# Optimization experiments

Measured on AMD Instinct MI355X. Metric: run time of the kernel, lower is better.

The kernel has to match this reference:

```python
import jax, jax.numpy as jnp
import numpy as np

VOCAB = 1_000_000
EMB = 64
HID = 200
BATCH = 16384
FIELDS = 50
EPS = 1e-5


def batchnorm(x, gamma, beta):
    # training-mode BatchNorm1d: batch statistics, biased variance
    mean = jnp.mean(x, axis=0, keepdims=True)
    var = jnp.var(x, axis=0, keepdims=True)
    return (x - mean) * jax.lax.rsqrt(var + EPS) * gamma + beta


def setup_inputs() -> dict:
    key = jax.random.key(0)
    ks = jax.random.split(key, 9)
    x = jax.random.randint(ks[0], (BATCH, FIELDS), 0, VOCAB)
    emb = jax.random.normal(ks[1], (VOCAB, EMB), dtype=jnp.float32) * 0.01
    w1 = jax.random.normal(ks[2], (EMB, HID), dtype=jnp.float32) * (1.0 / np.sqrt(EMB))
    b1 = jnp.zeros((HID,), dtype=jnp.float32)
    w_last = jax.random.normal(ks[3], (HID, 1), dtype=jnp.float32) * (1.0 / np.sqrt(HID))
    b_last = jnp.zeros((1,), dtype=jnp.float32)
    g_bi = jnp.ones((EMB,), dtype=jnp.float32)
    be_bi = jnp.zeros((EMB,), dtype=jnp.float32)
    g_h = jnp.ones((HID,), dtype=jnp.float32)
    be_h = jnp.zeros((HID,), dtype=jnp.float32)
    return {"x": x, "emb": emb, "w1": w1, "b1": b1, "w_last": w_last,
            "b_last": b_last, "g_bi": g_bi, "be_bi": be_bi, "g_h": g_h, "be_h": be_h}


def reference(x, emb, w1, b1, w_last, b_last, g_bi, be_bi, g_h, be_h):
    e = emb[x]                                # [B, F, E] gather
    # sum_{i<j} e_i * e_j == 0.5 * ((sum e)^2 - sum e^2)  (FM identity)
    s = jnp.sum(e, axis=1)                    # [B, E]
    sq = jnp.sum(e * e, axis=1)               # [B, E]
    bi = 0.5 * (s * s - sq)                   # [B, E]
    h = jax.nn.relu(batchnorm(bi, g_bi, be_bi))
    # single fc layer (layers=1); dropout is identity in eval mode
    h = jax.nn.relu(batchnorm(h @ w1 + b1, g_h, be_h))
    out = jax.nn.sigmoid(h @ w_last + b_last)  # [B, 1]
    return out
```

## Files before the change

### kernel.cpp

```cpp
#include <hip/hip_runtime.h>
#include <hip/hip_bf16.h>

#define BATCH 16384
#define FIELDS 50
#define EMB 64
#define HID 200
#define NCOPY 16

__global__ __launch_bounds__(256) void k_fm(const int* __restrict__ x,
                                            const float* __restrict__ emb,
                                            float* __restrict__ bi,
                                            float* __restrict__ st1) {
    __shared__ int sidx[16 * FIELDS];
    __shared__ float swave[4][128];
    const int tid = threadIdx.x;
    for (int i = tid; i < 16 * FIELDS; i += 256)
        sidx[i] = x[blockIdx.x * 16 * FIELDS + i];
    __syncthreads();

    const int r = tid >> 4;
    const int c = tid & 15;
    const int* rowidx = sidx + r * FIELDS;

    float s0 = 0.f, s1 = 0.f, s2 = 0.f, s3 = 0.f;
    float q0 = 0.f, q1 = 0.f, q2 = 0.f, q3 = 0.f;
#pragma unroll 10
    for (int f = 0; f < FIELDS; ++f) {
        const float4 v = *(const float4*)(emb + (size_t)rowidx[f] * EMB + c * 4);
        s0 += v.x; q0 += v.x * v.x;
        s1 += v.y; q1 += v.y * v.y;
        s2 += v.z; q2 += v.z * v.z;
        s3 += v.w; q3 += v.w * v.w;
    }
    float4 o;
    o.x = 0.5f * (s0 * s0 - q0);
    o.y = 0.5f * (s1 * s1 - q1);
    o.z = 0.5f * (s2 * s2 - q2);
    o.w = 0.5f * (s3 * s3 - q3);
    const int row = blockIdx.x * 16 + r;
    *(float4*)(bi + row * EMB + c * 4) = o;

    float pv0 = o.x, pv1 = o.y, pv2 = o.z, pv3 = o.w;
    float pq0 = o.x * o.x, pq1 = o.y * o.y, pq2 = o.z * o.z, pq3 = o.w * o.w;
#pragma unroll
    for (int off = 16; off <= 32; off <<= 1) {
        pv0 += __shfl_xor(pv0, off, 64); pq0 += __shfl_xor(pq0, off, 64);
        pv1 += __shfl_xor(pv1, off, 64); pq1 += __shfl_xor(pq1, off, 64);
        pv2 += __shfl_xor(pv2, off, 64); pq2 += __shfl_xor(pq2, off, 64);
        pv3 += __shfl_xor(pv3, off, 64); pq3 += __shfl_xor(pq3, off, 64);
    }
    const int lane = tid & 63;
    const int w = tid >> 6;
    if (lane < 16) {
        float4* sv = (float4*)&swave[w][lane * 4];
        float4* sq = (float4*)&swave[w][64 + lane * 4];
        *sv = make_float4(pv0, pv1, pv2, pv3);
        *sq = make_float4(pq0, pq1, pq2, pq3);
    }
    __syncthreads();
    if (tid < 128) {
        float t = swave[0][tid] + swave[1][tid] + swave[2][tid] + swave[3][tid];
        atomicAdd(st1 + (blockIdx.x & (NCOPY - 1)) * 128 + tid, t);
    }
}

__global__ __launch_bounds__(256) void k_fc1(const float* __restrict__ bi,
                                             const float* __restrict__ st1,
                                             const float* __restrict__ g_bi,
                                             const float* __restrict__ be_bi,
                                             const float* __restrict__ w1,
                                             const float* __restrict__ b1,
                                             float* __restrict__ y,
                                             float* __restrict__ st2) {
    __shared__ float w1s[EMB * HID + 64];
    __shared__ float b1s[HID];
    __shared__ float c1s[128];
    const int tid = threadIdx.x;
    for (int i = tid; i < EMB * HID; i += 256) w1s[i] = w1[i];
    if (tid < 64) w1s[EMB * HID + tid] = 0.f;
    if (tid < HID) b1s[tid] = b1[tid];
    if (tid < 64) {
        float s = 0.f, q = 0.f;
        for (int cc = 0; cc < NCOPY; ++cc) {
            s += st1[cc * 128 + tid];
            q += st1[cc * 128 + 64 + tid];
        }
        float mean = s * (1.f / BATCH);
        float var = q * (1.f / BATCH) - mean * mean;
        float a = g_bi[tid] * rsqrtf(var + 1e-5f);
        c1s[tid] = a;
        c1s[64 + tid] = be_bi[tid] - mean * a;
    }
    __syncthreads();

    const int l = tid & 63;
    const int w = tid >> 6;
    const float a1 = c1s[l];
    const float c1v = c1s[64 + l];
    const int base_row = blockIdx.x * 32 + w * 8;

    float z[8];
#pragma unroll
    for (int r = 0; r < 8; ++r) {
        float v = bi[(base_row + r) * EMB + l];
        v = a1 * v + c1v;
        z[r] = v > 0.f ? v : 0.f;
    }

    float acc[8][4];
#pragma unroll
    for (int r = 0; r < 8; ++r)
#pragma unroll
        for (int k = 0; k < 4; ++k) acc[r][k] = 0.f;

#pragma unroll 8
    for (int d = 0; d < EMB; ++d) {
        float w0 = w1s[d * HID + l];
        float wv1 = w1s[d * HID + 64 + l];
        float w2 = w1s[d * HID + 128 + l];
        float w3 = w1s[d * HID + 192 + l];
#pragma unroll
        for (int r = 0; r < 8; ++r) {
            float zz = __int_as_float(
                __builtin_amdgcn_readlane(__float_as_int(z[r]), d));
            acc[r][0] += zz * w0;
            acc[r][1] += zz * wv1;
            acc[r][2] += zz * w2;
            acc[r][3] += zz * w3;
        }
    }

    float s0 = 0.f, s1 = 0.f, s2 = 0.f, s3 = 0.f;
    float q0 = 0.f, q1 = 0.f, q2 = 0.f, q3 = 0.f;
    const float bb0 = b1s[l], bb1 = b1s[64 + l], bb2 = b1s[128 + l];
    const float bb3 = (l < 8) ? b1s[192 + l] : 0.f;
#pragma unroll
    for (int r = 0; r < 8; ++r) {
        int row = base_row + r;
        float v0 = acc[r][0] + bb0;
        float v1 = acc[r][1] + bb1;
        float v2 = acc[r][2] + bb2;
        y[row * HID + l] = v0;
        y[row * HID + 64 + l] = v1;
        y[row * HID + 128 + l] = v2;
        s0 += v0; q0 += v0 * v0;
        s1 += v1; q1 += v1 * v1;
        s2 += v2; q2 += v2 * v2;
        if (l < 8) {
            float v3 = acc[r][3] + bb3;
            y[row * HID + 192 + l] = v3;
            s3 += v3; q3 += v3 * v3;
        }
    }
    float* st = st2 + (blockIdx.x & (NCOPY - 1)) * 400;
    atomicAdd(st + l, s0);
    atomicAdd(st + 200 + l, q0);
    atomicAdd(st + 64 + l, s1);
    atomicAdd(st + 200 + 64 + l, q1);
    atomicAdd(st + 128 + l, s2);
    atomicAdd(st + 200 + 128 + l, q2);
    if (l < 8) {
        atomicAdd(st + 192 + l, s3);
        atomicAdd(st + 200 + 192 + l, q3);
    }
}

__global__ __launch_bounds__(256) void k_out(const float* __restrict__ y,
                                             const float* __restrict__ st2,
                                             const float* __restrict__ g_h,
                                             const float* __restrict__ be_h,
                                             const float* __restrict__ wl,
                                             const float* __restrict__ bl,
                                             float* __restrict__ out) {
    __shared__ float c2s[400];
    const int tid = threadIdx.x;
    if (tid < HID) {
        float s = 0.f, q = 0.f;
        for (int cc = 0; cc < NCOPY; ++cc) {
            s += st2[cc * 400 + tid];
            q += st2[cc * 400 + 200 + tid];
        }
        float mean = s * (1.f / BATCH);
        float var = q * (1.f / BATCH) - mean * mean;
        float a = g_h[tid] * rsqrtf(var + 1e-5f);
        c2s[tid] = a;
        c2s[200 + tid] = be_h[tid] - mean * a;
    }
    __syncthreads();

    const int l = tid & 63;
    const int w = tid >> 6;
    const int j0 = l, j1 = 64 + l, j2 = 128 + l;
    const int j3 = (l < 8) ? (192 + l) : 199;
    const float a0 = c2s[j0], c0 = c2s[200 + j0];
    const float a1 = c2s[j1], c1 = c2s[200 + j1];
    const float a2 = c2s[j2], c2 = c2s[200 + j2];
    const float a3 = c2s[j3], c3 = c2s[200 + j3];
    const float w0 = wl[j0], w1v = wl[j1], w2 = wl[j2], w3 = wl[j3];
    const float blv = bl[0];

#pragma unroll
    for (int it = 0; it < 4; ++it) {
        int row = blockIdx.x * 16 + it * 4 + w;
        const float* yr = y + row * HID;
        float v0 = a0 * yr[j0] + c0;
        float v1 = a1 * yr[j1] + c1;
        float v2 = a2 * yr[j2] + c2;
        float v3 = a3 * yr[j3] + c3;
        v0 = v0 > 0.f ? v0 : 0.f;
        v1 = v1 > 0.f ? v1 : 0.f;
        v2 = v2 > 0.f ? v2 : 0.f;
        v3 = v3 > 0.f ? v3 : 0.f;
        float t = v0 * w0 + v1 * w1v + v2 * w2 + ((l < 8) ? v3 * w3 : 0.f);
#pragma unroll
        for (int off = 32; off > 0; off >>= 1) t += __shfl_xor(t, off, 64);
        if (l == 0) out[row] = 1.f / (1.f + __expf(-(t + blv)));
    }
}

extern "C" void kernel_launch(void* const* d_in, const int* in_sizes, int n_in,
                              void* d_out, int out_size, void* d_ws, size_t ws_size,
                              hipStream_t stream) {
    const int* x = (const int*)d_in[0];
    const float* emb = (const float*)d_in[1];
    const float* w1 = (const float*)d_in[2];
    const float* b1 = (const float*)d_in[3];
    const float* wl = (const float*)d_in[4];
    const float* bl = (const float*)d_in[5];
    const float* g_bi = (const float*)d_in[6];
    const float* be_bi = (const float*)d_in[7];
    const float* g_h = (const float*)d_in[8];
    const float* be_h = (const float*)d_in[9];
    float* out = (float*)d_out;

    float* ws = (float*)d_ws;
    float* bi = ws;
    float* y = bi + BATCH * EMB;
    float* st1 = y + (size_t)BATCH * HID;
    float* st2 = st1 + NCOPY * 128;

    hipMemsetAsync(st1, 0, (NCOPY * 128 + NCOPY * 400) * sizeof(float), stream);

    k_fm<<<BATCH / 16, 256, 0, stream>>>(x, emb, bi, st1);
    k_fc1<<<BATCH / 32, 256, 0, stream>>>(bi, st1, g_bi, be_bi, w1, b1, y, st2);
    k_out<<<BATCH / 16, 256, 0, stream>>>(y, st2, g_h, be_h, wl, bl, out);
}
```

Measured before the change: 67.67 us.

## Fuse FM, FC1 and output stages into one cooperative kernel with grid syncs

Replaces the three kernels with a single cooperative kernel of 512 blocks, each handling 32 rows. Batchnorm statistics are exchanged through two grid-wide syncs, and the intermediate bi and y activations stay in shared memory and registers instead of making round trips through global memory. This removes two kernel launches and the y write/read traffic. In exchange, the w1 staging into shared memory (about 51KB) limits occupancy during the gather phase, and cooperative grid sync has its own cost.

```diff
diff --git a/kernel.cpp b/kernel.cpp
--- a/kernel.cpp
+++ b/kernel.cpp
@@ -1,47 +1,70 @@
 #include <hip/hip_runtime.h>
 #include <hip/hip_bf16.h>
+#include <hip/hip_cooperative_groups.h>
+
+namespace cg = cooperative_groups;
 
 #define BATCH 16384
 #define FIELDS 50
 #define EMB 64
 #define HID 200
 #define NCOPY 16
-
-__global__ __launch_bounds__(256) void k_fm(const int* __restrict__ x,
-                                            const float* __restrict__ emb,
-                                            float* __restrict__ bi,
-                                            float* __restrict__ st1) {
-    __shared__ int sidx[16 * FIELDS];
+#define GRID 512
+#define RPB 32
+
+__global__ __launch_bounds__(256, 2) void k_fused(
+    const int* __restrict__ x, const float* __restrict__ emb,
+    const float* __restrict__ w1, const float* __restrict__ b1,
+    const float* __restrict__ wl, const float* __restrict__ bl,
+    const float* __restrict__ g_bi, const float* __restrict__ be_bi,
+    const float* __restrict__ g_h, const float* __restrict__ be_h,
+    float* __restrict__ out, float* __restrict__ st1, float* __restrict__ st2)
+{
+    __shared__ int sidx[RPB * FIELDS];
+    __shared__ float sbi[RPB][EMB];
+    __shared__ float w1s[EMB * HID + 64];
+    __shared__ float b1s[HID];
+    __shared__ float c1s[128];
+    __shared__ float c2s[400];
     __shared__ float swave[4][128];
+
     const int tid = threadIdx.x;
-    for (int i = tid; i < 16 * FIELDS; i += 256)
-        sidx[i] = x[blockIdx.x * 16 * FIELDS + i];
+    const int bid = blockIdx.x;
+    const int row0 = bid * RPB;
+    const int lane = tid & 63;
+    const int w = tid >> 6;
+
+    for (int i = tid; i < RPB * FIELDS; i += 256)
+        sidx[i] = x[row0 * FIELDS + i];
     __syncthreads();
 
     const int r = tid >> 4;
     const int c = tid & 15;
-    const int* rowidx = sidx + r * FIELDS;
-
-    float s0 = 0.f, s1 = 0.f, s2 = 0.f, s3 = 0.f;
-    float q0 = 0.f, q1 = 0.f, q2 = 0.f, q3 = 0.f;
+    float pv0 = 0, pv1 = 0, pv2 = 0, pv3 = 0;
+    float pq0 = 0, pq1 = 0, pq2 = 0, pq3 = 0;
+#pragma unroll
+    for (int g = 0; g < 2; ++g) {
+        const int* rowidx = sidx + (g * 16 + r) * FIELDS;
+        float s0 = 0, s1 = 0, s2 = 0, s3 = 0, q0 = 0, q1 = 0, q2 = 0, q3 = 0;
 #pragma unroll 10
-    for (int f = 0; f < FIELDS; ++f) {
-        const float4 v = *(const float4*)(emb + (size_t)rowidx[f] * EMB + c * 4);
-        s0 += v.x; q0 += v.x * v.x;
-        s1 += v.y; q1 += v.y * v.y;
-        s2 += v.z; q2 += v.z * v.z;
-        s3 += v.w; q3 += v.w * v.w;
-    }
-    float4 o;
-    o.x = 0.5f * (s0 * s0 - q0);
-    o.y = 0.5f * (s1 * s1 - q1);
-    o.z = 0.5f * (s2 * s2 - q2);
-    o.w = 0.5f * (s3 * s3 - q3);
-    const int row = blockIdx.x * 16 + r;
-    *(float4*)(bi + row * EMB + c * 4) = o;
-
-    float pv0 = o.x, pv1 = o.y, pv2 = o.z, pv3 = o.w;
-    float pq0 = o.x * o.x, pq1 = o.y * o.y, pq2 = o.z * o.z, pq3 = o.w * o.w;
+        for (int f = 0; f < FIELDS; ++f) {
+            const float4 v = *(const float4*)(emb + (size_t)rowidx[f] * EMB + c * 4);
+            s0 += v.x; q0 += v.x * v.x;
+            s1 += v.y; q1 += v.y * v.y;
+            s2 += v.z; q2 += v.z * v.z;
+            s3 += v.w; q3 += v.w * v.w;
+        }
+        float4 o;
+        o.x = 0.5f * (s0 * s0 - q0);
+        o.y = 0.5f * (s1 * s1 - q1);
+        o.z = 0.5f * (s2 * s2 - q2);
+        o.w = 0.5f * (s3 * s3 - q3);
+        *(float4*)(&sbi[g * 16 + r][c * 4]) = o;
+        pv0 += o.x; pq0 += o.x * o.x;
+        pv1 += o.y; pq1 += o.y * o.y;
+        pv2 += o.z; pq2 += o.z * o.z;
+        pv3 += o.w; pq3 += o.w * o.w;
+    }
 #pragma unroll
     for (int off = 16; off <= 32; off <<= 1) {
         pv0 += __shfl_xor(pv0, off, 64); pq0 += __shfl_xor(pq0, off, 64);
@@ -49,38 +72,24 @@
         pv2 += __shfl_xor(pv2, off, 64); pq2 += __shfl_xor(pq2, off, 64);
         pv3 += __shfl_xor(pv3, off, 64); pq3 += __shfl_xor(pq3, off, 64);
     }
-    const int lane = tid & 63;
-    const int w = tid >> 6;
     if (lane < 16) {
-        float4* sv = (float4*)&swave[w][lane * 4];
-        float4* sq = (float4*)&swave[w][64 + lane * 4];
-        *sv = make_float4(pv0, pv1, pv2, pv3);
-        *sq = make_float4(pq0, pq1, pq2, pq3);
+        *(float4*)&swave[w][lane * 4] = make_float4(pv0, pv1, pv2, pv3);
+        *(float4*)&swave[w][64 + lane * 4] = make_float4(pq0, pq1, pq2, pq3);
     }
     __syncthreads();
     if (tid < 128) {
         float t = swave[0][tid] + swave[1][tid] + swave[2][tid] + swave[3][tid];
-        atomicAdd(st1 + (blockIdx.x & (NCOPY - 1)) * 128 + tid, t);
-    }
-}
-
-__global__ __launch_bounds__(256) void k_fc1(const float* __restrict__ bi,
-                                             const float* __restrict__ st1,
-                                             const float* __restrict__ g_bi,
-                                             const float* __restrict__ be_bi,
-                                             const float* __restrict__ w1,
-                                             const float* __restrict__ b1,
-                                             float* __restrict__ y,
-                                             float* __restrict__ st2) {
-    __shared__ float w1s[EMB * HID + 64];
-    __shared__ float b1s[HID];
-    __shared__ float c1s[128];
-    const int tid = threadIdx.x;
+        atomicAdd(st1 + (bid & (NCOPY - 1)) * 128 + tid, t);
+    }
+
     for (int i = tid; i < EMB * HID; i += 256) w1s[i] = w1[i];
     if (tid < 64) w1s[EMB * HID + tid] = 0.f;
     if (tid < HID) b1s[tid] = b1[tid];
+
+    cg::this_grid().sync();
+
     if (tid < 64) {
-        float s = 0.f, q = 0.f;
+        float s = 0, q = 0;
         for (int cc = 0; cc < NCOPY; ++cc) {
             s += st1[cc * 128 + tid];
             q += st1[cc * 128 + 64 + tid];
@@ -93,25 +102,20 @@
     }
     __syncthreads();
 
-    const int l = tid & 63;
-    const int w = tid >> 6;
-    const float a1 = c1s[l];
-    const float c1v = c1s[64 + l];
-    const int base_row = blockIdx.x * 32 + w * 8;
-
+    const int l = lane;
+    const float a1 = c1s[l], c1v = c1s[64 + l];
     float z[8];
 #pragma unroll
-    for (int r = 0; r < 8; ++r) {
-        float v = bi[(base_row + r) * EMB + l];
+    for (int rr = 0; rr < 8; ++rr) {
+        float v = sbi[w * 8 + rr][l];
         v = a1 * v + c1v;
-        z[r] = v > 0.f ? v : 0.f;
-    }
-
+        z[rr] = v > 0.f ? v : 0.f;
+    }
     float acc[8][4];
 #pragma unroll
-    for (int r = 0; r < 8; ++r)
-#pragma unroll
-        for (int k = 0; k < 4; ++k) acc[r][k] = 0.f;
+    for (int rr = 0; rr < 8; ++rr)
+#pragma unroll
+        for (int k = 0; k < 4; ++k) acc[rr][k] = 0.f;
 
 #pragma unroll 8
     for (int d = 0; d < EMB; ++d) {
@@ -120,62 +124,40 @@
         float w2 = w1s[d * HID + 128 + l];
         float w3 = w1s[d * HID + 192 + l];
 #pragma unroll
-        for (int r = 0; r < 8; ++r) {
+        for (int rr = 0; rr < 8; ++rr) {
             float zz = __int_as_float(
-                __builtin_amdgcn_readlane(__float_as_int(z[r]), d));
-            acc[r][0] += zz * w0;
-            acc[r][1] += zz * wv1;
-            acc[r][2] += zz * w2;
-            acc[r][3] += zz * w3;
-        }
-    }
-
-    float s0 = 0.f, s1 = 0.f, s2 = 0.f, s3 = 0.f;
-    float q0 = 0.f, q1 = 0.f, q2 = 0.f, q3 = 0.f;
+                __builtin_amdgcn_readlane(__float_as_int(z[rr]), d));
+            acc[rr][0] += zz * w0;
+            acc[rr][1] += zz * wv1;
+            acc[rr][2] += zz * w2;
+            acc[rr][3] += zz * w3;
+        }
+    }
+
+    float s0 = 0, s1 = 0, s2 = 0, s3 = 0, q0 = 0, q1 = 0, q2 = 0, q3 = 0;
     const float bb0 = b1s[l], bb1 = b1s[64 + l], bb2 = b1s[128 + l];
     const float bb3 = (l < 8) ? b1s[192 + l] : 0.f;
 #pragma unroll
-    for (int r = 0; r < 8; ++r) {
-        int row = base_row + r;
-        float v0 = acc[r][0] + bb0;
-        float v1 = acc[r][1] + bb1;
-        float v2 = acc[r][2] + bb2;
-        y[row * HID + l] = v0;
-        y[row * HID + 64 + l] = v1;
-        y[row * HID + 128 + l] = v2;
-        s0 += v0; q0 += v0 * v0;
-        s1 += v1; q1 += v1 * v1;
-        s2 += v2; q2 += v2 * v2;
-        if (l < 8) {
-            float v3 = acc[r][3] + bb3;
-            y[row * HID + 192 + l] = v3;
-            s3 += v3; q3 += v3 * v3;
-        }
-    }
-    float* st = st2 + (blockIdx.x & (NCOPY - 1)) * 400;
-    atomicAdd(st + l, s0);
-    atomicAdd(st + 200 + l, q0);
-    atomicAdd(st + 64 + l, s1);
-    atomicAdd(st + 200 + 64 + l, q1);
-    atomicAdd(st + 128 + l, s2);
-    atomicAdd(st + 200 + 128 + l, q2);
-    if (l < 8) {
-        atomicAdd(st + 192 + l, s3);
-        atomicAdd(st + 200 + 192 + l, q3);
-    }
-}
-
-__global__ __launch_bounds__(256) void k_out(const float* __restrict__ y,
-                                             const float* __restrict__ st2,
-                                             const float* __restrict__ g_h,
-                                             const float* __restrict__ be_h,
-                                             const float* __restrict__ wl,
-                                             const float* __restrict__ bl,
-                                             float* __restrict__ out) {
-    __shared__ float c2s[400];
-    const int tid = threadIdx.x;
+    for (int rr = 0; rr < 8; ++rr) {
+        acc[rr][0] += bb0; acc[rr][1] += bb1;
+        acc[rr][2] += bb2; acc[rr][3] += bb3;
+        s0 += acc[rr][0]; q0 += acc[rr][0] * acc[rr][0];
+        s1 += acc[rr][1]; q1 += acc[rr][1] * acc[rr][1];
+        s2 += acc[rr][2]; q2 += acc[rr][2] * acc[rr][2];
+        if (l < 8) { s3 += acc[rr][3]; q3 += acc[rr][3] * acc[rr][3]; }
+    }
+    {
+        float* st = st2 + (bid & (NCOPY - 1)) * 400;
+        atomicAdd(st + l, s0);        atomicAdd(st + 200 + l, q0);
+        atomicAdd(st + 64 + l, s1);   atomicAdd(st + 200 + 64 + l, q1);
+        atomicAdd(st + 128 + l, s2);  atomicAdd(st + 200 + 128 + l, q2);
+        if (l < 8) { atomicAdd(st + 192 + l, s3); atomicAdd(st + 200 + 192 + l, q3); }
+    }
+
+    cg::this_grid().sync();
+
     if (tid < HID) {
-        float s = 0.f, q = 0.f;
+        float s = 0, q = 0;
         for (int cc = 0; cc < NCOPY; ++cc) {
             s += st2[cc * 400 + tid];
             q += st2[cc * 400 + 200 + tid];
@@ -188,33 +170,29 @@
     }
     __syncthreads();
 
-    const int l = tid & 63;
-    const int w = tid >> 6;
     const int j0 = l, j1 = 64 + l, j2 = 128 + l;
     const int j3 = (l < 8) ? (192 + l) : 199;
-    const float a0 = c2s[j0], c0 = c2s[200 + j0];
-    const float a1 = c2s[j1], c1 = c2s[200 + j1];
-    const float a2 = c2s[j2], c2 = c2s[200 + j2];
-    const float a3 = c2s[j3], c3 = c2s[200 + j3];
-    const float w0 = wl[j0], w1v = wl[j1], w2 = wl[j2], w3 = wl[j3];
+    const float A0 = c2s[j0], C0 = c2s[200 + j0];
+    const float A1 = c2s[j1], C1 = c2s[200 + j1];
+    const float A2 = c2s[j2], C2 = c2s[200 + j2];
+    const float A3 = c2s[j3], C3 = c2s[200 + j3];
+    const float W0 = wl[j0], W1v = wl[j1], W2 = wl[j2], W3 = wl[j3];
     const float blv = bl[0];
 
 #pragma unroll
-    for (int it = 0; it < 4; ++it) {
-        int row = blockIdx.x * 16 + it * 4 + w;
-        const float* yr = y + row * HID;
-        float v0 = a0 * yr[j0] + c0;
-        float v1 = a1 * yr[j1] + c1;
-        float v2 = a2 * yr[j2] + c2;
-        float v3 = a3 * yr[j3] + c3;
+    for (int rr = 0; rr < 8; ++rr) {
+        float v0 = A0 * acc[rr][0] + C0;
+        float v1 = A1 * acc[rr][1] + C1;
+        float v2 = A2 * acc[rr][2] + C2;
+        float v3 = A3 * acc[rr][3] + C3;
         v0 = v0 > 0.f ? v0 : 0.f;
         v1 = v1 > 0.f ? v1 : 0.f;
         v2 = v2 > 0.f ? v2 : 0.f;
         v3 = v3 > 0.f ? v3 : 0.f;
-        float t = v0 * w0 + v1 * w1v + v2 * w2 + ((l < 8) ? v3 * w3 : 0.f);
+        float t = v0 * W0 + v1 * W1v + v2 * W2 + ((l < 8) ? v3 * W3 : 0.f);
 #pragma unroll
         for (int off = 32; off > 0; off >>= 1) t += __shfl_xor(t, off, 64);
-        if (l == 0) out[row] = 1.f / (1.f + __expf(-(t + blv)));
+        if (l == 0) out[row0 + w * 8 + rr] = 1.f / (1.f + __expf(-(t + blv)));
     }
 }
 
@@ -233,15 +211,13 @@
     const float* be_h = (const float*)d_in[9];
     float* out = (float*)d_out;
 
-    float* ws = (float*)d_ws;
-    float* bi = ws;
-    float* y = bi + BATCH * EMB;
-    float* st1 = y + (size_t)BATCH * HID;
+    float* st1 = (float*)d_ws;
     float* st2 = st1 + NCOPY * 128;
 
-    hipMemsetAsync(st1, 0, (NCOPY * 128 + NCOPY * 400) * sizeof(float), stream);
-
-    k_fm<<<BATCH / 16, 256, 0, stream>>>(x, emb, bi, st1);
-    k_fc1<<<BATCH / 32, 256, 0, stream>>>(bi, st1, g_bi, be_bi, w1, b1, y, st2);
-    k_out<<<BATCH / 16, 256, 0, stream>>>(y, st2, g_h, be_h, wl, bl, out);
+    hipMemsetAsync(d_ws, 0, (NCOPY * 128 + NCOPY * 400) * sizeof(float), stream);
+
+    void* args[] = {(void*)&x, (void*)&emb, (void*)&w1, (void*)&b1,
+                    (void*)&wl, (void*)&bl, (void*)&g_bi, (void*)&be_bi,
+                    (void*)&g_h, (void*)&be_h, (void*)&out, (void*)&st1, (void*)&st2};
+    hipLaunchCooperativeKernel((void*)k_fused, dim3(GRID), dim3(256), args, 0, stream);
 }
```

New measurement: 172.8 us. 2.55x slower.
